# Optimization experiments

Hardware: AMD Instinct MI355X
Metric: run time of the kernel (lower is better)

Reference implementation:

```python
import jax, jax.numpy as jnp
import numpy as np

V, D, K, O, H = 20000, 256, 16, 128, 4
NEG_INF = -1e9


def setup_inputs() -> dict:
    key = jax.random.key(0)
    k1, k2, k3, k4 = jax.random.split(key, 4)
    x = jax.random.normal(k1, (V, D), dtype=jnp.float32)
    # padded adjacency list; value V (== mask_index) marks padding slots
    adj_lst = jax.random.randint(k2, (V, K), 0, V + 1, dtype=jnp.int64)
    W = jax.random.normal(k3, (H, D, O), dtype=jnp.float32) * 0.05  # per-head linear
    a = jax.random.normal(k4, (H, O), dtype=jnp.float32) * 0.05     # per-head attn vec
    b = jnp.zeros((H, O), dtype=jnp.float32)                         # per-head bias
    return {"x": x, "W": W, "a": a, "b": b, "adj_lst": adj_lst, "mask_index": V}


def reference(x, W, a, b, adj_lst, mask_index):
    # per-head linear transform: [H, V, O]
    t = jnp.einsum('vd,hdo->hvo', x, W)
    # per-node attention logits: [H, V]
    attn = jnp.einsum('hvo,ho->hv', t, a)
    pad = adj_lst == mask_index                      # [V, K] padding mask
    safe_idx = jnp.clip(adj_lst, 0, mask_index - 1)  # in-range gather indices
    # masked gather of neighbor attention logits: [H, V, K]
    scores = jnp.where(pad[None], NEG_INF, attn[:, safe_idx])
    coefs = jax.nn.softmax(scores, axis=-1)          # [H, V, K]
    # gather neighbor features and zero padded slots: [H, V, K, O]
    nbr = jnp.where(pad[None, :, :, None], 0.0, t[:, safe_idx])
    head = jnp.einsum('hvk,hvko->hvo', coefs, nbr) + b[:, None, :]
    out = jnp.mean(head, axis=0)                     # 1/H * add_n(heads)
    return jax.nn.relu(out)
```

## Files before the change

kernel.cpp:

```cpp
#include <hip/hip_runtime.h>


#define V_N 20000
#define D_N 256
#define K_N 16
#define O_N 128
#define H_N 4
#define NEG_INF -1e9f
#define TM 16

typedef _Float16 f16x8 __attribute__((ext_vector_type(8)));
typedef _Float16 f16x4 __attribute__((ext_vector_type(4)));
typedef float    f32x4 __attribute__((ext_vector_type(4)));

__global__ __launch_bounds__(256) void prep_kernel(
    const float* __restrict__ W, const float* __restrict__ a,
    _Float16* __restrict__ Wt, float* __restrict__ wt)
{
    if (blockIdx.x < 64) {
        const int idx  = blockIdx.x * 256 + threadIdx.x;
        const int lane = idx & 63;
        const int nt   = (idx >> 6) & 7;
        const int s    = (idx >> 9) & 7;
        const int h    = idx >> 12;
        const int o    = nt * 16 + (lane & 15);
        const int d0   = s * 32 + (lane >> 4) * 8;
        f16x8 v;
        #pragma unroll
        for (int j = 0; j < 8; ++j)
            v[j] = (_Float16)W[((size_t)h * D_N + d0 + j) * O_N + o];
        *(f16x8*)&Wt[(size_t)idx * 8] = v;
    } else {
        const int h = blockIdx.x - 64;
        const int d = threadIdx.x;
        const float* Wrow = W + ((size_t)h * D_N + d) * O_N;
        const float* ah   = a + h * O_N;
        float s = 0.f;
        #pragma unroll
        for (int o = 0; o < O_N; o += 4) {
            const float4 wv = *(const float4*)&Wrow[o];
            const float4 av = *(const float4*)&ah[o];
            s = fmaf(wv.x, av.x, s); s = fmaf(wv.y, av.y, s);
            s = fmaf(wv.z, av.z, s); s = fmaf(wv.w, av.w, s);
        }
        wt[h * D_N + d] = s;
    }
}

__global__ __launch_bounds__(256) void xsplit_attn_kernel(
    const float* __restrict__ x, const float* __restrict__ wt,
    _Float16* __restrict__ xh, float* __restrict__ attn4)
{
    const int wid  = threadIdx.x >> 6;
    const int lane = threadIdx.x & 63;
    const int v    = blockIdx.x * 4 + wid;

    const float4 p = *(const float4*)&x[(size_t)v * D_N + lane * 4];
    f16x4 hv = { (_Float16)p.x, (_Float16)p.y, (_Float16)p.z, (_Float16)p.w };
    *(f16x4*)&xh[(size_t)v * D_N + lane * 4] = hv;

    float s[H_N];
    #pragma unroll
    for (int h = 0; h < H_N; ++h) {
        const float4 w = *(const float4*)&wt[h * D_N + lane * 4];
        float t = fmaf(p.x, w.x, 0.f);
        t = fmaf(p.y, w.y, t); t = fmaf(p.z, w.z, t); t = fmaf(p.w, w.w, t);
        s[h] = t;
    }
    #pragma unroll
    for (int h = 0; h < H_N; ++h)
        #pragma unroll
        for (int dd = 32; dd >= 1; dd >>= 1)
            s[h] += __shfl_xor(s[h], dd);
    if (lane == 0)
        *(float4*)&attn4[(size_t)v * 4] = make_float4(s[0], s[1], s[2], s[3]);
}

__global__ __launch_bounds__(256, 4) void gat_kernel(
    const _Float16* __restrict__ xh, const float* __restrict__ attn4,
    const _Float16* __restrict__ Wt, const float* __restrict__ b,
    const int* __restrict__ adj, const int* __restrict__ mask_p,
    float* __restrict__ out)
{
    const int v0  = blockIdx.x * TM;
    const int tid = threadIdx.x;

    __shared__ int      sidx_s[TM][17];
    __shared__ float    coefs_s[K_N][17][H_N];
    __shared__ _Float16 yl[H_N * 512 * 8];

    {
        const int node = tid >> 4;
        const int k    = tid & 15;
        const int mask = mask_p[0];
        const int idx  = adj[(v0 + node) * K_N + k];
        const bool pad = (idx >= mask);
        const int safe = pad ? 0 : idx;
        const float4 av = *(const float4*)&attn4[(size_t)safe * 4];
        const float lg[H_N] = { pad ? NEG_INF : av.x, pad ? NEG_INF : av.y,
                                pad ? NEG_INF : av.z, pad ? NEG_INF : av.w };
        float c[H_N];
        #pragma unroll
        for (int h = 0; h < H_N; ++h) {
            float m = lg[h];
            #pragma unroll
            for (int s = 8; s >= 1; s >>= 1)
                m = fmaxf(m, __shfl_xor(m, s, 16));
            const float e = pad ? 0.f : __expf(lg[h] - m);
            float sum = e;
            #pragma unroll
            for (int s = 8; s >= 1; s >>= 1)
                sum += __shfl_xor(sum, s, 16);
            c[h] = pad ? 0.f : e / sum;
        }
        *(float4*)&coefs_s[k][node][0] = make_float4(c[0], c[1], c[2], c[3]);
        sidx_s[node][k] = safe;
    }
    __syncthreads();

    const int wid  = tid >> 6;
    const int lane = tid & 63;

    {
        const int hw = lane >> 5;
        const int sl = lane & 31;
        const _Float16* xsl = xh + sl * 8;

        f16x8 y[2][H_N];
        #pragma unroll
        for (int i = 0; i < 2; ++i)
            #pragma unroll
            for (int h = 0; h < H_N; ++h)
                #pragma unroll
                for (int j = 0; j < 8; ++j) y[i][h][j] = (_Float16)0.f;

        #pragma unroll 4
        for (int k = 0; k < K_N; ++k) {
            #pragma unroll
            for (int i = 0; i < 2; ++i) {
                const int n  = wid * 4 + 2 * i + hw;
                const int si = sidx_s[n][k];
                const f16x8 xv = *(const f16x8*)&xsl[(size_t)si * D_N];
                const float4 c = *(const float4*)&coefs_s[k][n][0];
                const _Float16 c0 = (_Float16)c.x, c1 = (_Float16)c.y,
                               c2 = (_Float16)c.z, c3 = (_Float16)c.w;
                y[i][0] += xv * c0;
                y[i][1] += xv * c1;
                y[i][2] += xv * c2;
                y[i][3] += xv * c3;
            }
        }
        #pragma unroll
        for (int i = 0; i < 2; ++i) {
            const int n    = wid * 4 + 2 * i + hw;
            const int slot = n * 32 + (sl ^ n);
            #pragma unroll
            for (int h = 0; h < H_N; ++h)
                *(f16x8*)&yl[(size_t)(h * 512 + slot) * 8] = y[i][h];
        }
    }
    __syncthreads();

    const int m = lane & 15;
    const int q = lane >> 4;
    f32x4 acc0 = (f32x4){0.f, 0.f, 0.f, 0.f};
    f32x4 acc1 = (f32x4){0.f, 0.f, 0.f, 0.f};
    {
        const _Float16* Wb = Wt + (size_t)lane * 8;
        #pragma unroll
        for (int h = 0; h < H_N; ++h) {
            #pragma unroll
            for (int s = 0; s < 8; ++s) {
                const int slot = m * 32 + ((s * 4 + q) ^ m);
                const f16x8 af = *(const f16x8*)&yl[(size_t)(h * 512 + slot) * 8];
                const size_t fb = (size_t)((h * 8 + s) * 8 + wid * 2) * 512;
                const f16x8 b0 = *(const f16x8*)&Wb[fb];
                const f16x8 b1 = *(const f16x8*)&Wb[fb + 512];
                acc0 = __builtin_amdgcn_mfma_f32_16x16x32_f16(af, b0, acc0, 0, 0, 0);
                acc1 = __builtin_amdgcn_mfma_f32_16x16x32_f16(af, b1, acc1, 0, 0, 0);
            }
        }
    }

    #pragma unroll
    for (int nt = 0; nt < 2; ++nt) {
        const f32x4 acc = nt ? acc1 : acc0;
        const int col = (wid * 2 + nt) * 16 + m;
        const float bb = b[col] + b[O_N + col] + b[2 * O_N + col] + b[3 * O_N + col];
        #pragma unroll
        for (int r = 0; r < 4; ++r) {
            const int node = q * 4 + r;
            out[(size_t)(v0 + node) * O_N + col] = fmaxf(0.25f * (acc[r] + bb), 0.f);
        }
    }
}

extern "C" void kernel_launch(void* const* d_in, const int* in_sizes, int n_in,
                              void* d_out, int out_size, void* d_ws, size_t ws_size,
                              hipStream_t stream) {
    const float* x      = (const float*)d_in[0];
    const float* W      = (const float*)d_in[1];
    const float* a      = (const float*)d_in[2];
    const float* b      = (const float*)d_in[3];
    const int*   adj    = (const int*)d_in[4];
    const int*   mask_p = (const int*)d_in[5];
    float*       out    = (float*)d_out;

    char* p = (char*)d_ws;
    float*    attn4 = (float*)p;
    _Float16* xh    = (_Float16*)(p + 320000);
    _Float16* Wt    = (_Float16*)(p + 10560000);
    float*    wt    = (float*)(p + 10822144);

    prep_kernel<<<68, 256, 0, stream>>>(W, a, Wt, wt);
    xsplit_attn_kernel<<<V_N / 4, 256, 0, stream>>>(x, wt, xh, attn4);
    gat_kernel<<<V_N / TM, 256, 0, stream>>>(xh, attn4, Wt, b, adj, mask_p, out);
}
```

Before: 118.3 us.

## Move x fp16 conversion into prep kernel and software-pipeline W fragment loads

The fp32-to-fp16 conversion of x now runs in the same launch as the weight preparation. The attention-logit pass becomes a separate kernel that reads the fp16 copy, so logits are computed from rounded x. In the main kernel, the first W fragments are loaded before the barrier and each step prefetches the next fragment, so global-load latency overlaps the MFMA chain. This hides load latency in the GEMM stage, but keeps three launches, adds an extra pass over xh, and slightly changes numerics.

```diff
diff --git a/kernel.cpp b/kernel.cpp
--- a/kernel.cpp
+++ b/kernel.cpp
@@ -13,11 +13,20 @@
 typedef _Float16 f16x4 __attribute__((ext_vector_type(4)));
 typedef float    f32x4 __attribute__((ext_vector_type(4)));
 
-__global__ __launch_bounds__(256) void prep_kernel(
+__global__ __launch_bounds__(256) void prep_all_kernel(
     const float* __restrict__ W, const float* __restrict__ a,
-    _Float16* __restrict__ Wt, float* __restrict__ wt)
+    const float* __restrict__ x,
+    _Float16* __restrict__ Wt, float* __restrict__ wt,
+    _Float16* __restrict__ xh)
 {
-    if (blockIdx.x < 64) {
+    if (blockIdx.x >= 68) {
+        const int wid  = threadIdx.x >> 6;
+        const int lane = threadIdx.x & 63;
+        const int v    = (blockIdx.x - 68) * 4 + wid;
+        const float4 p = *(const float4*)&x[(size_t)v * D_N + lane * 4];
+        f16x4 hv = { (_Float16)p.x, (_Float16)p.y, (_Float16)p.z, (_Float16)p.w };
+        *(f16x4*)&xh[(size_t)v * D_N + lane * 4] = hv;
+    } else if (blockIdx.x < 64) {
         const int idx  = blockIdx.x * 256 + threadIdx.x;
         const int lane = idx & 63;
         const int nt   = (idx >> 6) & 7;
@@ -47,24 +56,24 @@
     }
 }
 
-__global__ __launch_bounds__(256) void xsplit_attn_kernel(
-    const float* __restrict__ x, const float* __restrict__ wt,
-    _Float16* __restrict__ xh, float* __restrict__ attn4)
+__global__ __launch_bounds__(256) void attn_kernel(
+    const _Float16* __restrict__ xh, const float* __restrict__ wt,
+    float* __restrict__ attn4)
 {
     const int wid  = threadIdx.x >> 6;
     const int lane = threadIdx.x & 63;
     const int v    = blockIdx.x * 4 + wid;
 
-    const float4 p = *(const float4*)&x[(size_t)v * D_N + lane * 4];
-    f16x4 hv = { (_Float16)p.x, (_Float16)p.y, (_Float16)p.z, (_Float16)p.w };
-    *(f16x4*)&xh[(size_t)v * D_N + lane * 4] = hv;
+    const f16x4 hv = *(const f16x4*)&xh[(size_t)v * D_N + lane * 4];
+    const float p0 = (float)hv[0], p1 = (float)hv[1],
+                p2 = (float)hv[2], p3 = (float)hv[3];
 
     float s[H_N];
     #pragma unroll
     for (int h = 0; h < H_N; ++h) {
         const float4 w = *(const float4*)&wt[h * D_N + lane * 4];
-        float t = fmaf(p.x, w.x, 0.f);
-        t = fmaf(p.y, w.y, t); t = fmaf(p.z, w.z, t); t = fmaf(p.w, w.w, t);
+        float t = fmaf(p0, w.x, 0.f);
+        t = fmaf(p1, w.y, t); t = fmaf(p2, w.z, t); t = fmaf(p3, w.w, t);
         s[h] = t;
     }
     #pragma unroll
@@ -120,6 +129,7 @@
 
     const int wid  = tid >> 6;
     const int lane = tid & 63;
+    const _Float16* Wb = Wt + (size_t)lane * 8 + (size_t)wid * 1024;
 
     {
         const int hw = lane >> 5;
@@ -159,27 +169,29 @@
                 *(f16x8*)&yl[(size_t)(h * 512 + slot) * 8] = y[i][h];
         }
     }
+
+    f16x8 cb0 = *(const f16x8*)&Wb[0];
+    f16x8 cb1 = *(const f16x8*)&Wb[512];
     __syncthreads();
 
     const int m = lane & 15;
     const int q = lane >> 4;
     f32x4 acc0 = (f32x4){0.f, 0.f, 0.f, 0.f};
     f32x4 acc1 = (f32x4){0.f, 0.f, 0.f, 0.f};
-    {
-        const _Float16* Wb = Wt + (size_t)lane * 8;
-        #pragma unroll
-        for (int h = 0; h < H_N; ++h) {
-            #pragma unroll
-            for (int s = 0; s < 8; ++s) {
-                const int slot = m * 32 + ((s * 4 + q) ^ m);
-                const f16x8 af = *(const f16x8*)&yl[(size_t)(h * 512 + slot) * 8];
-                const size_t fb = (size_t)((h * 8 + s) * 8 + wid * 2) * 512;
-                const f16x8 b0 = *(const f16x8*)&Wb[fb];
-                const f16x8 b1 = *(const f16x8*)&Wb[fb + 512];
-                acc0 = __builtin_amdgcn_mfma_f32_16x16x32_f16(af, b0, acc0, 0, 0, 0);
-                acc1 = __builtin_amdgcn_mfma_f32_16x16x32_f16(af, b1, acc1, 0, 0, 0);
-            }
-        }
+    #pragma unroll
+    for (int f = 0; f < 32; ++f) {
+        f16x8 nb0, nb1;
+        if (f < 31) {
+            nb0 = *(const f16x8*)&Wb[(size_t)(f + 1) * 4096];
+            nb1 = *(const f16x8*)&Wb[(size_t)(f + 1) * 4096 + 512];
+        }
+        const int h    = f >> 3;
+        const int s    = f & 7;
+        const int slot = m * 32 + ((s * 4 + q) ^ m);
+        const f16x8 af = *(const f16x8*)&yl[(size_t)(h * 512 + slot) * 8];
+        acc0 = __builtin_amdgcn_mfma_f32_16x16x32_f16(af, cb0, acc0, 0, 0, 0);
+        acc1 = __builtin_amdgcn_mfma_f32_16x16x32_f16(af, cb1, acc1, 0, 0, 0);
+        cb0 = nb0; cb1 = nb1;
     }
 
     #pragma unroll
@@ -212,7 +224,7 @@
     _Float16* Wt    = (_Float16*)(p + 10560000);
     float*    wt    = (float*)(p + 10822144);
 
-    prep_kernel<<<68, 256, 0, stream>>>(W, a, Wt, wt);
-    xsplit_attn_kernel<<<V_N / 4, 256, 0, stream>>>(x, wt, xh, attn4);
+    prep_all_kernel<<<68 + V_N / 4, 256, 0, stream>>>(W, a, x, Wt, wt, xh);
+    attn_kernel<<<V_N / 4, 256, 0, stream>>>(xh, wt, attn4);
     gat_kernel<<<V_N / TM, 256, 0, stream>>>(xh, attn4, Wt, b, adj, mask_p, out);
 }
```

Result: no change. 116.1 us (-1.9%).
